# Kernel tuning notes

Hardware: AMD Instinct MI355X
Metric: run time of the kernel (lower is better)

## Reference

```python
import jax, jax.numpy as jnp
import numpy as np

B, N, C, H = 4, 1024, 768, 12
D = C // H  # head_dim = 64
EPS_BN = 1e-5


def setup_inputs() -> dict:
    key = jax.random.key(0)
    ks = jax.random.split(key, 8)
    s = np.float32(D ** -0.5)
    return {
        "x": jax.random.normal(ks[0], (B, N, C), dtype=jnp.float32),
        "qkv_w": jax.random.normal(ks[1], (3 * C, C), dtype=jnp.float32) * (C ** -0.5),
        "qkv_b": jnp.zeros((3 * C,), dtype=jnp.float32),
        "proj_w": jax.random.normal(ks[2], (C, C), dtype=jnp.float32) * (C ** -0.5),
        "proj_b": jnp.zeros((C,), dtype=jnp.float32),
        "scale": jnp.asarray(s),
        "riem_scale": jnp.asarray(s),
        "grass_scale": jnp.asarray(s),
        "conv_w": jax.random.normal(ks[3], (H, 3 * H), dtype=jnp.float32) * ((3 * H) ** -0.5),
        "conv_b": jnp.zeros((H,), dtype=jnp.float32),
        "bn_gamma": jnp.ones((H,), dtype=jnp.float32),
        "bn_beta": jnp.zeros((H,), dtype=jnp.float32),
        "bn_mean": jnp.zeros((H,), dtype=jnp.float32),
        "bn_var": jnp.ones((H,), dtype=jnp.float32),
    }


def reference(x, qkv_w, qkv_b, proj_w, proj_b, scale, riem_scale, grass_scale,
              conv_w, conv_b, bn_gamma, bn_beta, bn_mean, bn_var):
    Bx, Nx, Cx = x.shape
    # qkv projection -> [3, B, H, N, D]
    qkv = (x @ qkv_w.T + qkv_b).reshape(Bx, Nx, 3, H, D).transpose(2, 0, 3, 1, 4)
    q, k, v = qkv[0], qkv[1], qkv[2]

    # Grassmannian points: reduced QR over each [N, D] token matrix
    qgr, _ = jnp.linalg.qr(q)
    kgr, _ = jnp.linalg.qr(k)
    # dots [B,H,N,N]; norm over singleton dim == abs, then squared -> dots**2
    dots = jnp.einsum('bhnd,bhmd->bhnm', qgr, kgr)
    attn_grass = (dots * dots) * grass_scale

    # standard scaled dot-product scores
    qk = jnp.einsum('bhnd,bhmd->bhnm', q, k)
    attn = qk * scale

    # covariance Frobenius distance between rank-1 covariances q_i q_i^T, k_j k_j^T:
    # ||q q^T - k k^T||_F^2 = |q|^4 + |k|^4 - 2 (q.k)^2 ; similarity = -sqrt(.)
    qn2 = jnp.sum(q * q, axis=-1)  # [B,H,N]
    kn2 = jnp.sum(k * k, axis=-1)  # [B,H,N]
    d2 = qn2[..., :, None] ** 2 + kn2[..., None, :] ** 2 - 2.0 * (qk * qk)
    attn_riem = -jnp.sqrt(jnp.maximum(d2, 0.0) + 1e-8) * riem_scale

    # concat over head-channel dim -> [B, 3H, N, N], 1x1 conv + BatchNorm (eval stats)
    cat = jnp.concatenate([attn, attn_riem, attn_grass], axis=1)
    y = jnp.einsum('bcnm,oc->bonm', cat, conv_w) + conv_b[None, :, None, None]
    inv = (bn_gamma / jnp.sqrt(bn_var + EPS_BN))[None, :, None, None]
    y = (y - bn_mean[None, :, None, None]) * inv + bn_beta[None, :, None, None]

    p = jax.nn.softmax(y, axis=-1)
    out = jnp.einsum('bhnm,bhmd->bhnd', p, v)  # [B,H,N,D]
    out = out.transpose(0, 2, 1, 3).reshape(Bx, Nx, Cx)
    return out @ proj_w.T + proj_b
```

## Files before the change

kernel.cpp:

```cpp
#include <hip/hip_runtime.h>
#include <math.h>


typedef __attribute__((ext_vector_type(8))) short short8;
typedef __attribute__((ext_vector_type(4))) float f32x4;

__device__ __forceinline__ unsigned bf16r(float x) {
    unsigned u = __float_as_uint(x);
    return (u + 0x7FFFu + ((u >> 16) & 1u)) >> 16;
}
__device__ __forceinline__ unsigned packhl(float x) {
    unsigned u = __float_as_uint(x);
    unsigned hi = (u + 0x7FFFu + ((u >> 16) & 1u)) & 0xFFFF0000u;
    float lo = x - __uint_as_float(hi);
    unsigned ul = __float_as_uint(lo);
    unsigned l16 = (ul + 0x7FFFu + ((ul >> 16) & 1u)) >> 16;
    return hi | (l16 & 0xFFFFu);
}
__device__ __forceinline__ float unpackhl(unsigned u) {
    return __uint_as_float(u & 0xFFFF0000u) + __uint_as_float(u << 16);
}
union U4S8 { uint4 u; short8 s; };
__device__ __forceinline__ short8 mk_hi(uint4 a, uint4 b) {
    U4S8 r;
    r.u.x = __builtin_amdgcn_perm(a.y, a.x, 0x07060302);
    r.u.y = __builtin_amdgcn_perm(a.w, a.z, 0x07060302);
    r.u.z = __builtin_amdgcn_perm(b.y, b.x, 0x07060302);
    r.u.w = __builtin_amdgcn_perm(b.w, b.z, 0x07060302);
    return r.s;
}
__device__ __forceinline__ short8 mk_lo(uint4 a, uint4 b) {
    U4S8 r;
    r.u.x = __builtin_amdgcn_perm(a.y, a.x, 0x05040100);
    r.u.y = __builtin_amdgcn_perm(a.w, a.z, 0x05040100);
    r.u.z = __builtin_amdgcn_perm(b.y, b.x, 0x05040100);
    r.u.w = __builtin_amdgcn_perm(b.w, b.z, 0x05040100);
    return r.s;
}
__device__ __forceinline__ uint4 ld4v(const unsigned* vp, int mbase, int d) {
    uint4 r;
    r.x = vp[(size_t)(mbase + 0) * 64 + d];
    r.y = vp[(size_t)(mbase + 1) * 64 + d];
    r.z = vp[(size_t)(mbase + 2) * 64 + d];
    r.w = vp[(size_t)(mbase + 3) * 64 + d];
    return r;
}
#define MFMA(a,b,c) __builtin_amdgcn_mfma_f32_16x16x32_bf16(a, b, c, 0, 0, 0)

__global__ __launch_bounds__(256) void pack_f32(
    const float* __restrict__ src, unsigned* __restrict__ dst, int n4)
{
    int i = blockIdx.x * 256 + threadIdx.x;
    if (i < n4) {
        float4 v = *(const float4*)&src[(size_t)i * 4];
        uint4 o;
        o.x = packhl(v.x); o.y = packhl(v.y); o.z = packhl(v.z); o.w = packhl(v.w);
        *(uint4*)&dst[(size_t)i * 4] = o;
    }
}

__global__ __launch_bounds__(256) void qkv_mfma(
    const unsigned* __restrict__ xpk, const unsigned* __restrict__ wpk,
    const float* __restrict__ bias,
    float* __restrict__ q, float* __restrict__ k,
    unsigned* __restrict__ qpk, unsigned* __restrict__ kpk, unsigned* __restrict__ vpk)
{
    __shared__ unsigned xT[32 * 64];
    __shared__ unsigned wT[64 * 64];
    const int tid = threadIdx.x;
    const int lane = tid & 63;
    const int w = tid >> 6;
    const int rowL = lane & 15;
    const int g = lane >> 4;
    const int r7 = rowL & 7;
    const int n0 = blockIdx.x * 64;
    const int m0 = blockIdx.y * 32;
    f32x4 accA = {0,0,0,0}, accB = {0,0,0,0};

    for (int kk0 = 0; kk0 < 768; kk0 += 64) {
        __syncthreads();
#pragma unroll
        for (int e = 0; e < 2; e++) {
            int ci = tid + 256 * e; int R = ci >> 4, c = ci & 15;
            uint4 v = *(const uint4*)&xpk[(size_t)(m0 + R) * 768 + kk0 + c * 4];
            *(uint4*)&xT[R * 64 + ((c ^ (R & 7)) << 2)] = v;
        }
#pragma unroll
        for (int e = 0; e < 4; e++) {
            int ci = tid + 256 * e; int R = ci >> 4, c = ci & 15;
            uint4 v = *(const uint4*)&wpk[(size_t)(n0 + R) * 768 + kk0 + c * 4];
            *(uint4*)&wT[R * 64 + ((c ^ (R & 7)) << 2)] = v;
        }
        __syncthreads();
#pragma unroll
        for (int ks = 0; ks < 2; ks++) {
            int c0 = ks * 8 + g * 2;
            uint4 b0 = *(const uint4*)&wT[(w * 16 + rowL) * 64 + ((c0 ^ r7) << 2)];
            uint4 b1 = *(const uint4*)&wT[(w * 16 + rowL) * 64 + (((c0 + 1) ^ r7) << 2)];
            short8 whi = mk_hi(b0, b1), wlo = mk_lo(b0, b1);
            uint4 a0 = *(const uint4*)&xT[rowL * 64 + ((c0 ^ r7) << 2)];
            uint4 a1 = *(const uint4*)&xT[rowL * 64 + (((c0 + 1) ^ r7) << 2)];
            short8 xhi = mk_hi(a0, a1), xlo = mk_lo(a0, a1);
            accA = MFMA(xhi, whi, accA);
            accA = MFMA(xhi, wlo, accA);
            accA = MFMA(xlo, whi, accA);
            uint4 a2 = *(const uint4*)&xT[(16 + rowL) * 64 + ((c0 ^ r7) << 2)];
            uint4 a3 = *(const uint4*)&xT[(16 + rowL) * 64 + (((c0 + 1) ^ r7) << 2)];
            short8 xhi2 = mk_hi(a2, a3), xlo2 = mk_lo(a2, a3);
            accB = MFMA(xhi2, whi, accB);
            accB = MFMA(xhi2, wlo, accB);
            accB = MFMA(xlo2, whi, accB);
        }
    }
    const int col = n0 + w * 16 + rowL;
    const float bv = bias[col];
    const int s = (n0 >= 1536) ? 2 : ((n0 >= 768) ? 1 : 0);
    const int hc = col - s * 768;
    const int head = hc >> 6;
    const int cin = hc & 63;
#pragma unroll
    for (int half = 0; half < 2; half++) {
        f32x4 acc = half ? accB : accA;
#pragma unroll
        for (int r = 0; r < 4; r++) {
            int row = m0 + half * 16 + g * 4 + r;
            int bb = row >> 10, n = row & 1023;
            size_t idx = ((size_t)(bb * 12 + head) << 16) + ((size_t)n << 6) + cin;
            float val = acc[r] + bv;
            if (s == 0)      { q[idx] = val; qpk[idx] = packhl(val); }
            else if (s == 1) { k[idx] = val; kpk[idx] = packhl(val); }
            else             { vpk[idx] = packhl(val); }
        }
    }
}

__global__ __launch_bounds__(256) void proj_mfma(
    const unsigned* __restrict__ apk, const unsigned* __restrict__ wpk,
    const float* __restrict__ bias, float* __restrict__ out)
{
    __shared__ unsigned xT[32 * 64];
    __shared__ unsigned wT[64 * 64];
    const int tid = threadIdx.x;
    const int lane = tid & 63;
    const int w = tid >> 6;
    const int rowL = lane & 15;
    const int g = lane >> 4;
    const int r7 = rowL & 7;
    const int n0 = blockIdx.x * 64;
    const int m0 = blockIdx.y * 32;
    f32x4 accA = {0,0,0,0}, accB = {0,0,0,0};

    for (int kk0 = 0; kk0 < 768; kk0 += 64) {
        __syncthreads();
#pragma unroll
        for (int e = 0; e < 2; e++) {
            int ci = tid + 256 * e; int R = ci >> 4, c = ci & 15;
            uint4 v = *(const uint4*)&apk[(size_t)(m0 + R) * 768 + kk0 + c * 4];
            *(uint4*)&xT[R * 64 + ((c ^ (R & 7)) << 2)] = v;
        }
#pragma unroll
        for (int e = 0; e < 4; e++) {
            int ci = tid + 256 * e; int R = ci >> 4, c = ci & 15;
            uint4 v = *(const uint4*)&wpk[(size_t)(n0 + R) * 768 + kk0 + c * 4];
            *(uint4*)&wT[R * 64 + ((c ^ (R & 7)) << 2)] = v;
        }
        __syncthreads();
#pragma unroll
        for (int ks = 0; ks < 2; ks++) {
            int c0 = ks * 8 + g * 2;
            uint4 b0 = *(const uint4*)&wT[(w * 16 + rowL) * 64 + ((c0 ^ r7) << 2)];
            uint4 b1 = *(const uint4*)&wT[(w * 16 + rowL) * 64 + (((c0 + 1) ^ r7) << 2)];
            short8 whi = mk_hi(b0, b1), wlo = mk_lo(b0, b1);
            uint4 a0 = *(const uint4*)&xT[rowL * 64 + ((c0 ^ r7) << 2)];
            uint4 a1 = *(const uint4*)&xT[rowL * 64 + (((c0 + 1) ^ r7) << 2)];
            short8 xhi = mk_hi(a0, a1), xlo = mk_lo(a0, a1);
            accA = MFMA(xhi, whi, accA);
            accA = MFMA(xhi, wlo, accA);
            accA = MFMA(xlo, whi, accA);
            uint4 a2 = *(const uint4*)&xT[(16 + rowL) * 64 + ((c0 ^ r7) << 2)];
            uint4 a3 = *(const uint4*)&xT[(16 + rowL) * 64 + (((c0 + 1) ^ r7) << 2)];
            short8 xhi2 = mk_hi(a2, a3), xlo2 = mk_lo(a2, a3);
            accB = MFMA(xhi2, whi, accB);
            accB = MFMA(xhi2, wlo, accB);
            accB = MFMA(xlo2, whi, accB);
        }
    }
    const int col = n0 + w * 16 + rowL;
    const float bv = bias[col];
#pragma unroll
    for (int half = 0; half < 2; half++) {
        f32x4 acc = half ? accB : accA;
#pragma unroll
        for (int r = 0; r < 4; r++) {
            int row = m0 + half * 16 + g * 4 + r;
            out[(size_t)row * 768 + col] = acc[r] + bv;
        }
    }
}

__global__ __launch_bounds__(256) void qkv_gemm(
    const float* __restrict__ x, const float* __restrict__ w, const float* __restrict__ bias,
    float* __restrict__ q, float* __restrict__ k,
    unsigned* __restrict__ qpk, unsigned* __restrict__ kpk, unsigned* __restrict__ vpk)
{
    __shared__ float As[16][68];
    __shared__ float Ws[16][68];
    const int tid = threadIdx.x;
    const int m0 = blockIdx.x * 64;
    const int c0 = blockIdx.y * 64;
    const int ty = tid >> 4, tx = tid & 15;
    const int lm = tid >> 2;
    const int lk = (tid & 3) * 4;
    float acc[4][4];
#pragma unroll
    for (int i = 0; i < 4; i++)
#pragma unroll
        for (int j = 0; j < 4; j++) acc[i][j] = 0.f;

    for (int kk0 = 0; kk0 < 768; kk0 += 16) {
        float4 av = *(const float4*)&x[(m0 + lm) * 768 + kk0 + lk];
        float4 wv = *(const float4*)&w[(c0 + lm) * 768 + kk0 + lk];
        __syncthreads();
        As[lk + 0][lm] = av.x; As[lk + 1][lm] = av.y; As[lk + 2][lm] = av.z; As[lk + 3][lm] = av.w;
        Ws[lk + 0][lm] = wv.x; Ws[lk + 1][lm] = wv.y; Ws[lk + 2][lm] = wv.z; Ws[lk + 3][lm] = wv.w;
        __syncthreads();
#pragma unroll
        for (int kk = 0; kk < 16; kk++) {
            float4 a  = *(const float4*)&As[kk][ty * 4];
            float4 bv = *(const float4*)&Ws[kk][tx * 4];
            acc[0][0] += a.x * bv.x; acc[0][1] += a.x * bv.y; acc[0][2] += a.x * bv.z; acc[0][3] += a.x * bv.w;
            acc[1][0] += a.y * bv.x; acc[1][1] += a.y * bv.y; acc[1][2] += a.y * bv.z; acc[1][3] += a.y * bv.w;
            acc[2][0] += a.z * bv.x; acc[2][1] += a.z * bv.y; acc[2][2] += a.z * bv.z; acc[2][3] += a.z * bv.w;
            acc[3][0] += a.w * bv.x; acc[3][1] += a.w * bv.y; acc[3][2] += a.w * bv.z; acc[3][3] += a.w * bv.w;
        }
    }
#pragma unroll
    for (int i = 0; i < 4; i++) {
        int row = m0 + ty * 4 + i;
        int bb = row >> 10, n = row & 1023;
#pragma unroll
        for (int j = 0; j < 4; j++) {
            int col = c0 + tx * 4 + j;
            float val = acc[i][j] + bias[col];
            int s = (col >= 1536) ? 2 : ((col >= 768) ? 1 : 0);
            int hc = col - s * 768;
            size_t idx = ((size_t)(bb * 12 + (hc >> 6)) << 16) + ((size_t)n << 6) + (hc & 63);
            if (s == 0)      { q[idx] = val; qpk[idx] = packhl(val); }
            else if (s == 1) { k[idx] = val; kpk[idx] = packhl(val); }
            else             { vpk[idx] = packhl(val); }
        }
    }
}

__global__ __launch_bounds__(256) void row_norms(
    const float* __restrict__ q, const float* __restrict__ k,
    float* __restrict__ qn4, float* __restrict__ kn4)
{
    int wid = blockIdx.x * 4 + (threadIdx.x >> 6);
    int lane = threadIdx.x & 63;
    const float* src; float* dst; int r;
    if (wid < 49152) { src = q; dst = qn4; r = wid; }
    else             { src = k; dst = kn4; r = wid - 49152; }
    float xv = src[(size_t)r * 64 + lane];
    float s = xv * xv;
#pragma unroll
    for (int m = 1; m < 64; m <<= 1) s += __shfl_xor(s, m, 64);
    if (lane == 0) dst[r] = s * s;
}

__global__ __launch_bounds__(1024)
__attribute__((amdgpu_waves_per_eu(4, 4)))
void qr_fact(const float* __restrict__ q, const float* __restrict__ k,
             unsigned* __restrict__ Vp_, float* __restrict__ taug)
{
    const int id = blockIdx.x;
    const float* src = (id & 1) ? k : q;
    src += (size_t)(id >> 1) << 16;
    unsigned* Vp = Vp_ + (size_t)id * 65536;
    const int tid = threadIdx.x;
    const int lane = tid & 63;
    const int w = tid >> 6;
    __shared__ float vbufA[1024];
    __shared__ float vbufB[1024];
    __shared__ float taub[64];

    float a[4][16];
#pragma unroll
    for (int c = 0; c < 4; c++)
#pragma unroll
        for (int i = 0; i < 16; i++)
            a[c][i] = src[(i * 64 + lane) * 64 + 4 * w + c];

    if (w == 0) {
        float part = 0.f;
#pragma unroll
        for (int i = 0; i < 16; i++) part += a[0][i] * a[0][i];
#pragma unroll
        for (int m = 1; m < 64; m <<= 1) part += __shfl_xor(part, m, 64);
        float sigma = part;
        float xd = __shfl(a[0][0], 0, 64);
        float nrm = sqrtf(sigma);
        float beta = (xd >= 0.f) ? -nrm : nrm;
        float vd = xd - beta;
        float vtv = (sigma - xd * xd) + vd * vd;
        float tau2 = (vtv > 0.f) ? 2.f / vtv : 0.f;
        if (lane == 0) a[0][0] = vd;
#pragma unroll
        for (int i = 0; i < 16; i++) vbufA[i * 64 + lane] = a[0][i];
        if (lane == 0) taub[0] = tau2;
    }
    __syncthreads();

    for (int d = 0; d < 64; d++) {
        float* vb = (d & 1) ? vbufB : vbufA;
        float vr[16];
#pragma unroll
        for (int i = 0; i < 16; i++) vr[i] = vb[i * 64 + lane];
        float t2 = taub[d];
        float dp0 = 0.f, dp1 = 0.f, dp2 = 0.f, dp3 = 0.f;
#pragma unroll
        for (int i = 0; i < 16; i++) {
            dp0 += vr[i] * a[0][i];
            dp1 += vr[i] * a[1][i];
            dp2 += vr[i] * a[2][i];
            dp3 += vr[i] * a[3][i];
        }
#pragma unroll
        for (int m = 1; m < 64; m <<= 1) {
            dp0 += __shfl_xor(dp0, m, 64);
            dp1 += __shfl_xor(dp1, m, 64);
            dp2 += __shfl_xor(dp2, m, 64);
            dp3 += __shfl_xor(dp3, m, 64);
        }
        const int jb = 4 * w;
        float s0 = t2 * dp0, s1 = t2 * dp1, s2 = t2 * dp2, s3 = t2 * dp3;
        if (jb + 0 > d) {
#pragma unroll
            for (int i = 0; i < 16; i++) a[0][i] -= s0 * vr[i];
        }
        if (jb + 1 > d) {
#pragma unroll
            for (int i = 0; i < 16; i++) a[1][i] -= s1 * vr[i];
        }
        if (jb + 2 > d) {
#pragma unroll
            for (int i = 0; i < 16; i++) a[2][i] -= s2 * vr[i];
        }
        if (jb + 3 > d) {
#pragma unroll
            for (int i = 0; i < 16; i++) a[3][i] -= s3 * vr[i];
        }
        if (d < 63) {
            const int dn = d + 1;
            if (w == (dn >> 2)) {
                const int cd = dn & 3;
#pragma unroll
                for (int c = 0; c < 4; c++) if (c == cd) {
                    float part = 0.f;
#pragma unroll
                    for (int i = 0; i < 16; i++) {
                        int r = i * 64 + lane;
                        float xx = a[c][i];
                        part += (r >= dn) ? xx * xx : 0.f;
                    }
#pragma unroll
                    for (int m = 1; m < 64; m <<= 1) part += __shfl_xor(part, m, 64);
                    float sigma = part;
                    float xd = __shfl(a[c][0], dn, 64);
                    float nrm = sqrtf(sigma);
                    float beta = (xd >= 0.f) ? -nrm : nrm;
                    float vd = xd - beta;
                    float vtv = (sigma - xd * xd) + vd * vd;
                    float tau2 = (vtv > 0.f) ? 2.f / vtv : 0.f;
                    if (lane == dn) a[c][0] = vd;
                    float* vbn = (dn & 1) ? vbufB : vbufA;
#pragma unroll
                    for (int i = 0; i < 16; i++) {
                        int r = i * 64 + lane;
                        vbn[i * 64 + lane] = (r < dn) ? 0.f : a[c][i];
                    }
                    if (lane == 0) taub[dn] = tau2;
                }
            }
        }
        __syncthreads();
    }

    if (tid < 64) taug[id * 64 + tid] = taub[tid];
#pragma unroll
    for (int c = 0; c < 4; c++) {
        int j = 4 * w + c;
#pragma unroll
        for (int i = 0; i < 16; i++) {
            int r = i * 64 + lane;
            float vv = (r < j) ? 0.f : a[c][i];
            Vp[(size_t)j * 1024 + r] = packhl(vv);
        }
    }
}

__global__ __launch_bounds__(256) void qr_gpart(
    const unsigned* __restrict__ Vp_, float* __restrict__ Gpart)
{
    const int id = blockIdx.x;
    const int sl = blockIdx.y;
    const unsigned* Vp = Vp_ + (size_t)id * 65536;
    __shared__ unsigned Vc[64 * 32];
    const int tid = threadIdx.x;
    const int lane = tid & 63;
    const int w = tid >> 6;
    const int rowL = lane & 15;
    const int g = lane >> 4;

    f32x4 acc0 = {0,0,0,0}, acc1 = {0,0,0,0}, acc2 = {0,0,0,0}, acc3 = {0,0,0,0};
    for (int r0 = sl * 256; r0 < sl * 256 + 256; r0 += 32) {
        __syncthreads();
#pragma unroll
        for (int e = 0; e < 2; e++) {
            int ci = tid + 256 * e;
            int row = ci >> 3, c = ci & 7;
            uint4 v = *(const uint4*)&Vp[(size_t)row * 1024 + r0 + c * 4];
            *(uint4*)&Vc[row * 32 + ((c ^ (row & 7)) << 2)] = v;
        }
        __syncthreads();
        int ra = w * 16 + rowL;
        uint4 a0 = *(const uint4*)&Vc[ra * 32 + (((g * 2) ^ (ra & 7)) << 2)];
        uint4 a1 = *(const uint4*)&Vc[ra * 32 + (((g * 2 + 1) ^ (ra & 7)) << 2)];
        short8 Ahi = mk_hi(a0, a1), Alo = mk_lo(a0, a1);
#define GDO(jt, accv) { int rb = jt * 16 + rowL; \
        uint4 b0 = *(const uint4*)&Vc[rb * 32 + (((g * 2) ^ (rb & 7)) << 2)]; \
        uint4 b1 = *(const uint4*)&Vc[rb * 32 + (((g * 2 + 1) ^ (rb & 7)) << 2)]; \
        short8 Bhi = mk_hi(b0, b1), Blo = mk_lo(b0, b1); \
        accv = MFMA(Ahi, Bhi, accv); accv = MFMA(Ahi, Blo, accv); accv = MFMA(Alo, Bhi, accv); }
        GDO(0, acc0) GDO(1, acc1) GDO(2, acc2) GDO(3, acc3)
#undef GDO
    }
    float* dst = Gpart + ((size_t)(id * 4 + sl) << 12);
#define GWR(jt, accv) { \
    dst[(w * 16 + g * 4 + 0) * 64 + jt * 16 + rowL] = accv[0]; \
    dst[(w * 16 + g * 4 + 1) * 64 + jt * 16 + rowL] = accv[1]; \
    dst[(w * 16 + g * 4 + 2) * 64 + jt * 16 + rowL] = accv[2]; \
    dst[(w * 16 + g * 4 + 3) * 64 + jt * 16 + rowL] = accv[3]; }
    GWR(0, acc0) GWR(1, acc1) GWR(2, acc2) GWR(3, acc3)
#undef GWR
}

__global__ __launch_bounds__(256) void qr_tw2(
    const unsigned* __restrict__ Vp_, const float* __restrict__ taug,
    const float* __restrict__ Gpart, float* __restrict__ Wg)
{
    const int id = blockIdx.x;
    const unsigned* Vp = Vp_ + (size_t)id * 65536;
    __shared__ float G_s[64 * 65];
    __shared__ float wbuf[64];
    __shared__ float tau_s[64];
    const int tid = threadIdx.x;
    if (tid < 64) tau_s[tid] = taug[id * 64 + tid];
    const float* Gp = Gpart + ((size_t)(id * 4) << 12);
#pragma unroll
    for (int e = 0; e < 16; e++) {
        int idx = tid + 256 * e;
        float sum = Gp[idx] + Gp[4096 + idx] + Gp[8192 + idx] + Gp[12288 + idx];
        G_s[(idx >> 6) * 65 + (idx & 63)] = sum;
    }
    const int i = tid >> 2;
    const int cq = tid & 3;
    float regA[16];
#pragma unroll
    for (int cc = 0; cc < 16; cc++)
        regA[cc] = unpackhl(Vp[(size_t)i * 1024 + cq * 16 + cc]);
    __syncthreads();
    for (int j = 63; j >= 0; j--) {
        if (i == j) {
            float tj = tau_s[j];
#pragma unroll
            for (int cc = 0; cc < 16; cc++) {
                regA[cc] *= tj;
                wbuf[cq * 16 + cc] = regA[cc];
            }
        }
        __syncthreads();
        if (i < j) {
            float gij = G_s[i * 65 + j];
#pragma unroll
            for (int cc = 0; cc < 16; cc++)
                regA[cc] = fmaf(-gij, wbuf[cq * 16 + cc], regA[cc]);
        }
        __syncthreads();
    }
#pragma unroll
    for (int cc = 0; cc < 16; cc++)
        Wg[(size_t)id * 4096 + i * 64 + cq * 16 + cc] = regA[cc];
}

__global__ __launch_bounds__(256) void qr_formq(
    const unsigned* __restrict__ Vp_, const float* __restrict__ Wg,
    unsigned short* __restrict__ qgrh, unsigned short* __restrict__ kgrh)
{
    const int id = blockIdx.x;
    const int rb = blockIdx.y;
    const unsigned* Vp = Vp_ + (size_t)id * 65536;
    const float* Wm = Wg + (size_t)id * 4096;
    unsigned short* dst = ((id & 1) ? kgrh : qgrh) + ((size_t)(id >> 1) << 16);
    __shared__ float Vl[64 * 65];
    __shared__ float Wl[64 * 64];
    const int tid = threadIdx.x;
    const int rbase = rb * 64;
#pragma unroll
    for (int e = 0; e < 16; e++) {
        int idx = tid + 256 * e;
        int j = idx >> 6, rl = idx & 63;
        Vl[rl * 65 + j] = unpackhl(Vp[(size_t)j * 1024 + rbase + rl]);
        Wl[idx] = Wm[idx];
    }
    __syncthreads();
    const int rl = tid >> 2;
    const int cg = (tid & 3) << 4;
    const int rglob = rbase + rl;
    unsigned short outv[16];
#pragma unroll
    for (int cc = 0; cc < 16; cc++) {
        int c = cg + cc;
        float s = (rglob == c) ? 1.f : 0.f;
        for (int j = 0; j < 64; j++) s -= Vl[rl * 65 + j] * Wl[j * 64 + c];
        outv[cc] = (unsigned short)bf16r(s);
    }
#pragma unroll
    for (int cc = 0; cc < 16; cc += 4)
        *(ushort4*)&dst[(size_t)rglob * 64 + cg + cc] = *(ushort4*)&outv[cc];
}

#define SC_EACH12(F) F(0) F(1) F(2) F(3) F(4) F(5) F(6) F(7) F(8) F(9) F(10) F(11)
#define SC_DECLY(o) float y##o##_0 = 0.f, y##o##_1 = 0.f, y##o##_2 = 0.f, y##o##_3 = 0.f;
#define SC_LOADC(o) const float cA##o = cw[o * 36 + h], \
                                cB##o = cw[o * 36 + 12 + h], \
                                cC##o = cw[o * 36 + 24 + h];
#define SC_CONV1(o,r) y##o##_##r = fmaf(cA##o, att, fmaf(cB##o, rie, fmaf(cC##o, gra, y##o##_##r)));
#define SC_CONVROW(r) SC_CONV1(0,r) SC_CONV1(1,r) SC_CONV1(2,r) SC_CONV1(3,r) SC_CONV1(4,r) SC_CONV1(5,r) \
                      SC_CONV1(6,r) SC_CONV1(7,r) SC_CONV1(8,r) SC_CONV1(9,r) SC_CONV1(10,r) SC_CONV1(11,r)
#define SC_SCORE(r) { \
    float qk = s1[r], gr = s2[r]; \
    float qn4v = qn4s[g * 4 + r]; \
    float att = qk * scale; \
    float d2 = qn4v + kn4v - 2.f * qk * qk; \
    float rie = -sqrtf(fmaxf(d2, 0.f) + 1e-8f) * riem_scale; \
    float gra = gr * gr * grass_scale; \
    SC_CONVROW(r) }
#define SC_OUT(o) { \
    float inv = bn_gamma[o] * rsqrtf(bn_var[o] + 1e-5f); \
    float Bb = fmaf(conv_b[o] - bn_mean[o], inv, bn_beta[o]); \
    float* dst = Sbuf + ((size_t)(z * 12 + o) * 1024 + n0) * 1024 + m0 + w * 16 + rowL; \
    dst[(size_t)(g * 4 + 0) * 1024] = fmaf(y##o##_0, inv, Bb); \
    dst[(size_t)(g * 4 + 1) * 1024] = fmaf(y##o##_1, inv, Bb); \
    dst[(size_t)(g * 4 + 2) * 1024] = fmaf(y##o##_2, inv, Bb); \
    dst[(size_t)(g * 4 + 3) * 1024] = fmaf(y##o##_3, inv, Bb); }

__global__ __launch_bounds__(256) void sattn_scores(
    const unsigned* __restrict__ qpk, const unsigned* __restrict__ kpk,
    const unsigned short* __restrict__ qgrh, const unsigned short* __restrict__ kgrh,
    const float* __restrict__ qn4g, const float* __restrict__ kn4g,
    const float* __restrict__ cw, const float* __restrict__ conv_b,
    const float* __restrict__ bn_gamma, const float* __restrict__ bn_beta,
    const float* __restrict__ bn_mean, const float* __restrict__ bn_var,
    const float* __restrict__ scale_p, const float* __restrict__ riem_p,
    const float* __restrict__ grass_p, float* __restrict__ Sbuf, int b0)
{
    __shared__ unsigned qT[16 * 64];
    __shared__ unsigned short qgT[16 * 64];
    __shared__ unsigned kL[64 * 64];
    __shared__ unsigned short kgrL[64 * 64];
    __shared__ float qn4s[16];
    __shared__ float kn4s[64];

    const int tid = threadIdx.x;
    const int lane = tid & 63;
    const int w = tid >> 6;
    const int rowL = lane & 15;
    const int g = lane >> 4;
    const int r7 = rowL & 7;
    const int m0 = blockIdx.x * 64;
    const int n0 = blockIdx.y * 16;
    const int z = blockIdx.z;
    const int b = b0 + z;
    const float scale = scale_p[0], riem_scale = riem_p[0], grass_scale = grass_p[0];

    SC_EACH12(SC_DECLY)

    for (int h = 0; h < 12; h++) {
        __syncthreads();
        {
            int R = tid >> 4, c = tid & 15;
            uint4 v = *(const uint4*)&qpk[((size_t)(b * 12 + h) << 16) + (size_t)(n0 + R) * 64 + c * 4];
            *(uint4*)&qT[R * 64 + ((c ^ (R & 7)) << 2)] = v;
        }
        if (tid < 128) {
            int R = tid >> 3, c = tid & 7;
            uint4 v = *(const uint4*)&qgrh[((size_t)(b * 12 + h) << 16) + (size_t)(n0 + R) * 64 + c * 8];
            *(uint4*)&qgT[R * 64 + ((c ^ (R & 7)) << 3)] = v;
        }
#pragma unroll
        for (int e = 0; e < 4; e++) {
            int ci = tid + 256 * e; int m = ci >> 4, c = ci & 15;
            uint4 v = *(const uint4*)&kpk[((size_t)(b * 12 + h) << 16) + (size_t)(m0 + m) * 64 + c * 4];
            *(uint4*)&kL[m * 64 + ((c ^ (m & 7)) << 2)] = v;
        }
#pragma unroll
        for (int e = 0; e < 2; e++) {
            int ci = tid + 256 * e; int m = ci >> 3, c = ci & 7;
            uint4 v = *(const uint4*)&kgrh[((size_t)(b * 12 + h) << 16) + (size_t)(m0 + m) * 64 + c * 8];
            *(uint4*)&kgrL[m * 64 + ((c ^ (m & 7)) << 3)] = v;
        }
        if (tid < 64) kn4s[tid] = kn4g[(size_t)(b * 12 + h) * 1024 + m0 + tid];
        if (tid < 16) qn4s[tid] = qn4g[(size_t)(b * 12 + h) * 1024 + n0 + tid];
        __syncthreads();

        float kn4v = kn4s[w * 16 + rowL];
        f32x4 s1 = {0,0,0,0}, s2 = {0,0,0,0};
#pragma unroll
        for (int ks = 0; ks < 2; ks++) {
            int c0 = ks * 8 + g * 2;
            uint4 a0 = *(const uint4*)&qT[rowL * 64 + ((c0 ^ r7) << 2)];
            uint4 a1 = *(const uint4*)&qT[rowL * 64 + (((c0 + 1) ^ r7) << 2)];
            uint4 b0v = *(const uint4*)&kL[(w * 16 + rowL) * 64 + ((c0 ^ r7) << 2)];
            uint4 b1v = *(const uint4*)&kL[(w * 16 + rowL) * 64 + (((c0 + 1) ^ r7) << 2)];
            short8 qhi = mk_hi(a0, a1), qlo = mk_lo(a0, a1);
            short8 khi = mk_hi(b0v, b1v), klo = mk_lo(b0v, b1v);
            s1 = MFMA(qhi, khi, s1);
            s1 = MFMA(qhi, klo, s1);
            s1 = MFMA(qlo, khi, s1);
            int cg = ks * 4 + g;
            short8 qg = *(const short8*)&qgT[rowL * 64 + ((cg ^ r7) << 3)];
            short8 kg2 = *(const short8*)&kgrL[(w * 16 + rowL) * 64 + ((cg ^ r7) << 3)];
            s2 = MFMA(qg, kg2, s2);
        }
        SC_EACH12(SC_LOADC)
        SC_SCORE(0) SC_SCORE(1) SC_SCORE(2) SC_SCORE(3)
    }
    SC_EACH12(SC_OUT)
}

__global__ __launch_bounds__(256) void sattn_pv(
    const unsigned* __restrict__ vpk, const float* __restrict__ Sbuf,
    void* __restrict__ attno_out, int b0, int packout)
{
    __shared__ unsigned short P_s[16 * 64];
    __shared__ unsigned vt_s[64 * 64];
    __shared__ float mrun[16], lrun[16], cos_[16];

    const int tid = threadIdx.x;
    const int lane = tid & 63;
    const int w = tid >> 6;
    const int rowL = lane & 15;
    const int g = lane >> 4;
    const int r7 = rowL & 7;
    const int n0 = blockIdx.x * 16;
    const int o = blockIdx.y;
    const int z = blockIdx.z;
    const int b = b0 + z;
    const int srow = tid >> 4;
    const int sc4 = (tid & 15) * 4;

    if (tid < 16) { mrun[tid] = -1e30f; lrun[tid] = 0.f; }
    f32x4 acc = {0,0,0,0};
    const float* Srow = Sbuf + ((size_t)(z * 12 + o) * 1024 + n0 + srow) * 1024;
    const unsigned* vp = vpk + ((size_t)(b * 12 + o) << 16);
    __syncthreads();

    for (int m0 = 0; m0 < 1024; m0 += 64) {
        float4 sv = *(const float4*)&Srow[m0 + sc4];
        float mx = fmaxf(fmaxf(sv.x, sv.y), fmaxf(sv.z, sv.w));
        mx = fmaxf(mx, __shfl_xor(mx, 1, 64));
        mx = fmaxf(mx, __shfl_xor(mx, 2, 64));
        mx = fmaxf(mx, __shfl_xor(mx, 4, 64));
        mx = fmaxf(mx, __shfl_xor(mx, 8, 64));
        float mo = mrun[srow];
        float mn = fmaxf(mo, mx);
        float co = expf(mo - mn);
        float p0 = expf(sv.x - mn), p1 = expf(sv.y - mn), p2 = expf(sv.z - mn), p3 = expf(sv.w - mn);
        unsigned u0 = bf16r(p0), u1 = bf16r(p1), u2 = bf16r(p2), u3 = bf16r(p3);
        {
            ushort4 pw = make_ushort4((unsigned short)u0, (unsigned short)u1,
                                      (unsigned short)u2, (unsigned short)u3);
            *(ushort4*)&P_s[srow * 64 + (((sc4 >> 3) ^ (srow & 7)) << 3) + (sc4 & 7)] = pw;
        }
        float ps = __uint_as_float(u0 << 16) + __uint_as_float(u1 << 16)
                 + __uint_as_float(u2 << 16) + __uint_as_float(u3 << 16);
        ps += __shfl_xor(ps, 1, 64); ps += __shfl_xor(ps, 2, 64);
        ps += __shfl_xor(ps, 4, 64); ps += __shfl_xor(ps, 8, 64);
        if ((lane & 15) == 0) {
            mrun[srow] = mn;
            cos_[srow] = co;
            lrun[srow] = lrun[srow] * co + ps;
        }
#pragma unroll
        for (int e = 0; e < 4; e++) {
            int d_ = tid & 63;
            int mb = (tid >> 6) * 4 + 16 * e;
            int mc = (tid >> 6) + 4 * e;
            uint4 v = ld4v(vp + (size_t)m0 * 64, mb, d_);
            *(uint4*)&vt_s[d_ * 64 + ((mc ^ (d_ & 15)) << 2)] = v;
        }
        __syncthreads();
        {
            float c0_ = cos_[g * 4 + 0], c1_ = cos_[g * 4 + 1];
            float c2_ = cos_[g * 4 + 2], c3_ = cos_[g * 4 + 3];
            acc[0] *= c0_; acc[1] *= c1_; acc[2] *= c2_; acc[3] *= c3_;
        }
        const int d_ = w * 16 + rowL;
        const unsigned* vrow = &vt_s[d_ * 64];
#pragma unroll
        for (int kk = 0; kk < 2; kk++) {
            int mc8 = kk * 4 + g;
            short8 pa = *(const short8*)&P_s[rowL * 64 + ((mc8 ^ r7) << 3)];
            int c0 = kk * 8 + g * 2;
            uint4 b0v = *(const uint4*)&vrow[((c0 ^ (d_ & 15)) << 2)];
            uint4 b1v = *(const uint4*)&vrow[(((c0 + 1) ^ (d_ & 15)) << 2)];
            short8 vh = mk_hi(b0v, b1v), vl = mk_lo(b0v, b1v);
            acc = MFMA(pa, vh, acc);
            acc = MFMA(pa, vl, acc);
        }
        __syncthreads();
    }
#pragma unroll
    for (int r = 0; r < 4; r++) {
        int row = g * 4 + r;
        size_t idx = ((size_t)(b * 1024 + n0 + row)) * 768 + o * 64 + w * 16 + rowL;
        float v = acc[r] / lrun[row];
        if (packout) ((unsigned*)attno_out)[idx] = packhl(v);
        else         ((float*)attno_out)[idx] = v;
    }
}

__global__ __launch_bounds__(256) void proj_gemm(
    const float* __restrict__ x, const float* __restrict__ w, const float* __restrict__ bias,
    float* __restrict__ out)
{
    __shared__ float As[16][68];
    __shared__ float Ws[16][68];
    const int tid = threadIdx.x;
    const int m0 = blockIdx.x * 64;
    const int c0 = blockIdx.y * 64;
    const int ty = tid >> 4, tx = tid & 15;
    const int lm = tid >> 2;
    const int lk = (tid & 3) * 4;
    float acc[4][4];
#pragma unroll
    for (int i = 0; i < 4; i++)
#pragma unroll
        for (int j = 0; j < 4; j++) acc[i][j] = 0.f;

    for (int kk0 = 0; kk0 < 768; kk0 += 16) {
        float4 av = *(const float4*)&x[(m0 + lm) * 768 + kk0 + lk];
        float4 wv = *(const float4*)&w[(c0 + lm) * 768 + kk0 + lk];
        __syncthreads();
        As[lk + 0][lm] = av.x; As[lk + 1][lm] = av.y; As[lk + 2][lm] = av.z; As[lk + 3][lm] = av.w;
        Ws[lk + 0][lm] = wv.x; Ws[lk + 1][lm] = wv.y; Ws[lk + 2][lm] = wv.z; Ws[lk + 3][lm] = wv.w;
        __syncthreads();
#pragma unroll
        for (int kk = 0; kk < 16; kk++) {
            float4 a  = *(const float4*)&As[kk][ty * 4];
            float4 bv = *(const float4*)&Ws[kk][tx * 4];
            acc[0][0] += a.x * bv.x; acc[0][1] += a.x * bv.y; acc[0][2] += a.x * bv.z; acc[0][3] += a.x * bv.w;
            acc[1][0] += a.y * bv.x; acc[1][1] += a.y * bv.y; acc[1][2] += a.y * bv.z; acc[1][3] += a.y * bv.w;
            acc[2][0] += a.z * bv.x; acc[2][1] += a.z * bv.y; acc[2][2] += a.z * bv.z; acc[2][3] += a.z * bv.w;
            acc[3][0] += a.w * bv.x; acc[3][1] += a.w * bv.y; acc[3][2] += a.w * bv.z; acc[3][3] += a.w * bv.w;
        }
    }
#pragma unroll
    for (int i = 0; i < 4; i++) {
        int row = m0 + ty * 4 + i;
#pragma unroll
        for (int j = 0; j < 4; j++) {
            int col = c0 + tx * 4 + j;
            out[(size_t)row * 768 + col] = acc[i][j] + bias[col];
        }
    }
}

extern "C" void kernel_launch(void* const* d_in, const int* in_sizes, int n_in,
                              void* d_out, int out_size, void* d_ws, size_t ws_size,
                              hipStream_t stream) {
    const float* x          = (const float*)d_in[0];
    const float* qkv_w      = (const float*)d_in[1];
    const float* qkv_b      = (const float*)d_in[2];
    const float* proj_w     = (const float*)d_in[3];
    const float* proj_b     = (const float*)d_in[4];
    const float* scale      = (const float*)d_in[5];
    const float* riem_scale = (const float*)d_in[6];
    const float* grass_scale= (const float*)d_in[7];
    const float* conv_w     = (const float*)d_in[8];
    const float* conv_b     = (const float*)d_in[9];
    const float* bn_gamma   = (const float*)d_in[10];
    const float* bn_beta    = (const float*)d_in[11];
    const float* bn_mean    = (const float*)d_in[12];
    const float* bn_var     = (const float*)d_in[13];
    float* out = (float*)d_out;

    float* q   = (float*)d_ws;
    float* k   = q + 3145728;
    unsigned* qpk = (unsigned*)(k + 3145728);
    unsigned* kpk = qpk + 3145728;
    unsigned* vpk = kpk + 3145728;
    unsigned short* qgrh = (unsigned short*)(vpk + 3145728);
    unsigned short* kgrh = qgrh + 3145728;
    float* qn4 = (float*)(kgrh + 3145728);
    float* kn4 = qn4 + 49152;
    float* attno = q;
    unsigned* attno_pk = (unsigned*)q;
    unsigned* ppk = (unsigned*)k;

    const size_t BASE = 75890688ull;
    const size_t SB1  = 50331648ull;
    float* Sbuf = (float*)((char*)d_ws + BASE);
    unsigned* xpk_ = (unsigned*)((char*)d_ws + BASE);
    unsigned* wpk_ = xpk_ + 3145728;
    unsigned* Vpk2 = (unsigned*)((char*)d_ws + BASE);
    float* Wg   = (float*)(Vpk2 + 96 * 65536);
    float* taug = Wg + 96 * 4096;
    float* Gpart = taug + 96 * 64;
    const bool havePk = (ws_size >= BASE + SB1);
    const bool full   = (ws_size >= BASE + 4 * SB1);

    if (havePk) {
        hipLaunchKernelGGL(pack_f32, dim3(3072), dim3(256), 0, stream, x, xpk_, 786432);
        hipLaunchKernelGGL(pack_f32, dim3(1728), dim3(256), 0, stream, qkv_w, wpk_, 442368);
        hipLaunchKernelGGL(qkv_mfma, dim3(36, 128), dim3(256), 0, stream,
                           xpk_, wpk_, qkv_b, q, k, qpk, kpk, vpk);
    } else {
        hipLaunchKernelGGL(qkv_gemm, dim3(64, 36), dim3(256), 0, stream,
                           x, qkv_w, qkv_b, q, k, qpk, kpk, vpk);
    }
    hipLaunchKernelGGL(row_norms, dim3(24576), dim3(256), 0, stream, q, k, qn4, kn4);

    hipLaunchKernelGGL(qr_fact, dim3(96), dim3(1024), 0, stream, q, k, Vpk2, taug);
    hipLaunchKernelGGL(qr_gpart, dim3(96, 4), dim3(256), 0, stream, Vpk2, Gpart);
    hipLaunchKernelGGL(qr_tw2, dim3(96), dim3(256), 0, stream, Vpk2, taug, Gpart, Wg);
    hipLaunchKernelGGL(qr_formq, dim3(96, 16), dim3(256), 0, stream, Vpk2, Wg, qgrh, kgrh);

    if (havePk)
        hipLaunchKernelGGL(pack_f32, dim3(576), dim3(256), 0, stream, proj_w, ppk, 147456);

    if (full) {
        hipLaunchKernelGGL(sattn_scores, dim3(16, 64, 4), dim3(256), 0, stream,
                           qpk, kpk, qgrh, kgrh, qn4, kn4, conv_w, conv_b,
                           bn_gamma, bn_beta, bn_mean, bn_var,
                           scale, riem_scale, grass_scale, Sbuf, 0);
        hipLaunchKernelGGL(sattn_pv, dim3(64, 12, 4), dim3(256), 0, stream,
                           vpk, Sbuf, (void*)attno_pk, 0, 1);
    } else {
        for (int b = 0; b < 4; b++) {
            hipLaunchKernelGGL(sattn_scores, dim3(16, 64, 1), dim3(256), 0, stream,
                               qpk, kpk, qgrh, kgrh, qn4, kn4, conv_w, conv_b,
                               bn_gamma, bn_beta, bn_mean, bn_var,
                               scale, riem_scale, grass_scale, Sbuf, b);
            hipLaunchKernelGGL(sattn_pv, dim3(64, 12, 1), dim3(256), 0, stream,
                               vpk, Sbuf, (void*)(havePk ? (void*)attno_pk : (void*)attno), b,
                               havePk ? 1 : 0);
        }
    }

    if (havePk) {
        hipLaunchKernelGGL(proj_mfma, dim3(12, 128), dim3(256), 0, stream,
                           attno_pk, ppk, proj_b, out);
    } else {
        hipLaunchKernelGGL(proj_gemm, dim3(64, 12), dim3(256), 0, stream,
                           attno, proj_w, proj_b, out);
    }
}
```

Baseline: 678.8 us.

## Fuse fp32-to-bf16 split packing into GEMM loads and skip finished QR columns

```diff
diff --git a/kernel.cpp b/kernel.cpp
--- a/kernel.cpp
+++ b/kernel.cpp
@@ -16,6 +16,11 @@
     unsigned ul = __float_as_uint(lo);
     unsigned l16 = (ul + 0x7FFFu + ((ul >> 16) & 1u)) >> 16;
     return hi | (l16 & 0xFFFFu);
+}
+__device__ __forceinline__ uint4 pack4(float4 v) {
+    uint4 o;
+    o.x = packhl(v.x); o.y = packhl(v.y); o.z = packhl(v.z); o.w = packhl(v.w);
+    return o;
 }
 __device__ __forceinline__ float unpackhl(unsigned u) {
     return __uint_as_float(u & 0xFFFF0000u) + __uint_as_float(u << 16);
@@ -47,20 +52,8 @@
 }
 #define MFMA(a,b,c) __builtin_amdgcn_mfma_f32_16x16x32_bf16(a, b, c, 0, 0, 0)
 
-__global__ __launch_bounds__(256) void pack_f32(
-    const float* __restrict__ src, unsigned* __restrict__ dst, int n4)
-{
-    int i = blockIdx.x * 256 + threadIdx.x;
-    if (i < n4) {
-        float4 v = *(const float4*)&src[(size_t)i * 4];
-        uint4 o;
-        o.x = packhl(v.x); o.y = packhl(v.y); o.z = packhl(v.z); o.w = packhl(v.w);
-        *(uint4*)&dst[(size_t)i * 4] = o;
-    }
-}
-
 __global__ __launch_bounds__(256) void qkv_mfma(
-    const unsigned* __restrict__ xpk, const unsigned* __restrict__ wpk,
+    const float* __restrict__ x, const float* __restrict__ wsrc,
     const float* __restrict__ bias,
     float* __restrict__ q, float* __restrict__ k,
     unsigned* __restrict__ qpk, unsigned* __restrict__ kpk, unsigned* __restrict__ vpk)
@@ -82,14 +75,14 @@
 #pragma unroll
         for (int e = 0; e < 2; e++) {
             int ci = tid + 256 * e; int R = ci >> 4, c = ci & 15;
-            uint4 v = *(const uint4*)&xpk[(size_t)(m0 + R) * 768 + kk0 + c * 4];
-            *(uint4*)&xT[R * 64 + ((c ^ (R & 7)) << 2)] = v;
+            float4 fv = *(const float4*)&x[(size_t)(m0 + R) * 768 + kk0 + c * 4];
+            *(uint4*)&xT[R * 64 + ((c ^ (R & 7)) << 2)] = pack4(fv);
         }
 #pragma unroll
         for (int e = 0; e < 4; e++) {
             int ci = tid + 256 * e; int R = ci >> 4, c = ci & 15;
-            uint4 v = *(const uint4*)&wpk[(size_t)(n0 + R) * 768 + kk0 + c * 4];
-            *(uint4*)&wT[R * 64 + ((c ^ (R & 7)) << 2)] = v;
+            float4 fv = *(const float4*)&wsrc[(size_t)(n0 + R) * 768 + kk0 + c * 4];
+            *(uint4*)&wT[R * 64 + ((c ^ (R & 7)) << 2)] = pack4(fv);
         }
         __syncthreads();
 #pragma unroll
@@ -135,7 +128,7 @@
 }
 
 __global__ __launch_bounds__(256) void proj_mfma(
-    const unsigned* __restrict__ apk, const unsigned* __restrict__ wpk,
+    const unsigned* __restrict__ apk, const float* __restrict__ wsrc,
     const float* __restrict__ bias, float* __restrict__ out)
 {
     __shared__ unsigned xT[32 * 64];
@@ -161,8 +154,8 @@
 #pragma unroll
         for (int e = 0; e < 4; e++) {
             int ci = tid + 256 * e; int R = ci >> 4, c = ci & 15;
-            uint4 v = *(const uint4*)&wpk[(size_t)(n0 + R) * 768 + kk0 + c * 4];
-            *(uint4*)&wT[R * 64 + ((c ^ (R & 7)) << 2)] = v;
+            float4 fv = *(const float4*)&wsrc[(size_t)(n0 + R) * 768 + kk0 + c * 4];
+            *(uint4*)&wT[R * 64 + ((c ^ (R & 7)) << 2)] = pack4(fv);
         }
         __syncthreads();
 #pragma unroll
@@ -198,60 +191,6 @@
     }
 }
 
-__global__ __launch_bounds__(256) void qkv_gemm(
-    const float* __restrict__ x, const float* __restrict__ w, const float* __restrict__ bias,
-    float* __restrict__ q, float* __restrict__ k,
-    unsigned* __restrict__ qpk, unsigned* __restrict__ kpk, unsigned* __restrict__ vpk)
-{
-    __shared__ float As[16][68];
-    __shared__ float Ws[16][68];
-    const int tid = threadIdx.x;
-    const int m0 = blockIdx.x * 64;
-    const int c0 = blockIdx.y * 64;
-    const int ty = tid >> 4, tx = tid & 15;
-    const int lm = tid >> 2;
-    const int lk = (tid & 3) * 4;
-    float acc[4][4];
-#pragma unroll
-    for (int i = 0; i < 4; i++)
-#pragma unroll
-        for (int j = 0; j < 4; j++) acc[i][j] = 0.f;
-
-    for (int kk0 = 0; kk0 < 768; kk0 += 16) {
-        float4 av = *(const float4*)&x[(m0 + lm) * 768 + kk0 + lk];
-        float4 wv = *(const float4*)&w[(c0 + lm) * 768 + kk0 + lk];
-        __syncthreads();
-        As[lk + 0][lm] = av.x; As[lk + 1][lm] = av.y; As[lk + 2][lm] = av.z; As[lk + 3][lm] = av.w;
-        Ws[lk + 0][lm] = wv.x; Ws[lk + 1][lm] = wv.y; Ws[lk + 2][lm] = wv.z; Ws[lk + 3][lm] = wv.w;
-        __syncthreads();
-#pragma unroll
-        for (int kk = 0; kk < 16; kk++) {
-            float4 a  = *(const float4*)&As[kk][ty * 4];
-            float4 bv = *(const float4*)&Ws[kk][tx * 4];
-            acc[0][0] += a.x * bv.x; acc[0][1] += a.x * bv.y; acc[0][2] += a.x * bv.z; acc[0][3] += a.x * bv.w;
-            acc[1][0] += a.y * bv.x; acc[1][1] += a.y * bv.y; acc[1][2] += a.y * bv.z; acc[1][3] += a.y * bv.w;
-            acc[2][0] += a.z * bv.x; acc[2][1] += a.z * bv.y; acc[2][2] += a.z * bv.z; acc[2][3] += a.z * bv.w;
-            acc[3][0] += a.w * bv.x; acc[3][1] += a.w * bv.y; acc[3][2] += a.w * bv.z; acc[3][3] += a.w * bv.w;
-        }
-    }
-#pragma unroll
-    for (int i = 0; i < 4; i++) {
-        int row = m0 + ty * 4 + i;
-        int bb = row >> 10, n = row & 1023;
-#pragma unroll
-        for (int j = 0; j < 4; j++) {
-            int col = c0 + tx * 4 + j;
-            float val = acc[i][j] + bias[col];
-            int s = (col >= 1536) ? 2 : ((col >= 768) ? 1 : 0);
-            int hc = col - s * 768;
-            size_t idx = ((size_t)(bb * 12 + (hc >> 6)) << 16) + ((size_t)n << 6) + (hc & 63);
-            if (s == 0)      { q[idx] = val; qpk[idx] = packhl(val); }
-            else if (s == 1) { k[idx] = val; kpk[idx] = packhl(val); }
-            else             { vpk[idx] = packhl(val); }
-        }
-    }
-}
-
 __global__ __launch_bounds__(256) void row_norms(
     const float* __restrict__ q, const float* __restrict__ k,
     float* __restrict__ qn4, float* __restrict__ kn4)
@@ -312,43 +251,45 @@
     __syncthreads();
 
     for (int d = 0; d < 64; d++) {
-        float* vb = (d & 1) ? vbufB : vbufA;
-        float vr[16];
-#pragma unroll
-        for (int i = 0; i < 16; i++) vr[i] = vb[i * 64 + lane];
-        float t2 = taub[d];
-        float dp0 = 0.f, dp1 = 0.f, dp2 = 0.f, dp3 = 0.f;
-#pragma unroll
-        for (int i = 0; i < 16; i++) {
-            dp0 += vr[i] * a[0][i];
-            dp1 += vr[i] * a[1][i];
-            dp2 += vr[i] * a[2][i];
-            dp3 += vr[i] * a[3][i];
-        }
-#pragma unroll
-        for (int m = 1; m < 64; m <<= 1) {
-            dp0 += __shfl_xor(dp0, m, 64);
-            dp1 += __shfl_xor(dp1, m, 64);
-            dp2 += __shfl_xor(dp2, m, 64);
-            dp3 += __shfl_xor(dp3, m, 64);
-        }
         const int jb = 4 * w;
-        float s0 = t2 * dp0, s1 = t2 * dp1, s2 = t2 * dp2, s3 = t2 * dp3;
-        if (jb + 0 > d) {
-#pragma unroll
-            for (int i = 0; i < 16; i++) a[0][i] -= s0 * vr[i];
-        }
-        if (jb + 1 > d) {
-#pragma unroll
-            for (int i = 0; i < 16; i++) a[1][i] -= s1 * vr[i];
-        }
-        if (jb + 2 > d) {
-#pragma unroll
-            for (int i = 0; i < 16; i++) a[2][i] -= s2 * vr[i];
-        }
         if (jb + 3 > d) {
-#pragma unroll
-            for (int i = 0; i < 16; i++) a[3][i] -= s3 * vr[i];
+            float* vb = (d & 1) ? vbufB : vbufA;
+            float vr[16];
+#pragma unroll
+            for (int i = 0; i < 16; i++) vr[i] = vb[i * 64 + lane];
+            float t2 = taub[d];
+            float dp0 = 0.f, dp1 = 0.f, dp2 = 0.f, dp3 = 0.f;
+#pragma unroll
+            for (int i = 0; i < 16; i++) {
+                dp0 += vr[i] * a[0][i];
+                dp1 += vr[i] * a[1][i];
+                dp2 += vr[i] * a[2][i];
+                dp3 += vr[i] * a[3][i];
+            }
+#pragma unroll
+            for (int m = 1; m < 64; m <<= 1) {
+                dp0 += __shfl_xor(dp0, m, 64);
+                dp1 += __shfl_xor(dp1, m, 64);
+                dp2 += __shfl_xor(dp2, m, 64);
+                dp3 += __shfl_xor(dp3, m, 64);
+            }
+            float s0 = t2 * dp0, s1 = t2 * dp1, s2 = t2 * dp2, s3 = t2 * dp3;
+            if (jb + 0 > d) {
+#pragma unroll
+                for (int i = 0; i < 16; i++) a[0][i] -= s0 * vr[i];
+            }
+            if (jb + 1 > d) {
+#pragma unroll
+                for (int i = 0; i < 16; i++) a[1][i] -= s1 * vr[i];
+            }
+            if (jb + 2 > d) {
+#pragma unroll
+                for (int i = 0; i < 16; i++) a[2][i] -= s2 * vr[i];
+            }
+            {
+#pragma unroll
+                for (int i = 0; i < 16; i++) a[3][i] -= s3 * vr[i];
+            }
         }
         if (d < 63) {
             const int dn = d + 1;
@@ -641,7 +582,7 @@
 
 __global__ __launch_bounds__(256) void sattn_pv(
     const unsigned* __restrict__ vpk, const float* __restrict__ Sbuf,
-    void* __restrict__ attno_out, int b0, int packout)
+    unsigned* __restrict__ attno_pk, int b0)
 {
     __shared__ unsigned short P_s[16 * 64];
     __shared__ unsigned vt_s[64 * 64];
@@ -725,55 +666,7 @@
     for (int r = 0; r < 4; r++) {
         int row = g * 4 + r;
         size_t idx = ((size_t)(b * 1024 + n0 + row)) * 768 + o * 64 + w * 16 + rowL;
-        float v = acc[r] / lrun[row];
-        if (packout) ((unsigned*)attno_out)[idx] = packhl(v);
-        else         ((float*)attno_out)[idx] = v;
-    }
-}
-
-__global__ __launch_bounds__(256) void proj_gemm(
-    const float* __restrict__ x, const float* __restrict__ w, const float* __restrict__ bias,
-    float* __restrict__ out)
-{
-    __shared__ float As[16][68];
-    __shared__ float Ws[16][68];
-    const int tid = threadIdx.x;
-    const int m0 = blockIdx.x * 64;
-    const int c0 = blockIdx.y * 64;
-    const int ty = tid >> 4, tx = tid & 15;
-    const int lm = tid >> 2;
-    const int lk = (tid & 3) * 4;
-    float acc[4][4];
-#pragma unroll
-    for (int i = 0; i < 4; i++)
-#pragma unroll
-        for (int j = 0; j < 4; j++) acc[i][j] = 0.f;
-
-    for (int kk0 = 0; kk0 < 768; kk0 += 16) {
-        float4 av = *(const float4*)&x[(m0 + lm) * 768 + kk0 + lk];
-        float4 wv = *(const float4*)&w[(c0 + lm) * 768 + kk0 + lk];
-        __syncthreads();
-        As[lk + 0][lm] = av.x; As[lk + 1][lm] = av.y; As[lk + 2][lm] = av.z; As[lk + 3][lm] = av.w;
-        Ws[lk + 0][lm] = wv.x; Ws[lk + 1][lm] = wv.y; Ws[lk + 2][lm] = wv.z; Ws[lk + 3][lm] = wv.w;
-        __syncthreads();
-#pragma unroll
-        for (int kk = 0; kk < 16; kk++) {
-            float4 a  = *(const float4*)&As[kk][ty * 4];
-            float4 bv = *(const float4*)&Ws[kk][tx * 4];
-            acc[0][0] += a.x * bv.x; acc[0][1] += a.x * bv.y; acc[0][2] += a.x * bv.z; acc[0][3] += a.x * bv.w;
-            acc[1][0] += a.y * bv.x; acc[1][1] += a.y * bv.y; acc[1][2] += a.y * bv.z; acc[1][3] += a.y * bv.w;
-            acc[2][0] += a.z * bv.x; acc[2][1] += a.z * bv.y; acc[2][2] += a.z * bv.z; acc[2][3] += a.z * bv.w;
-            acc[3][0] += a.w * bv.x; acc[3][1] += a.w * bv.y; acc[3][2] += a.w * bv.z; acc[3][3] += a.w * bv.w;
-        }
-    }
-#pragma unroll
-    for (int i = 0; i < 4; i++) {
-        int row = m0 + ty * 4 + i;
-#pragma unroll
-        for (int j = 0; j < 4; j++) {
-            int col = c0 + tx * 4 + j;
-            out[(size_t)row * 768 + col] = acc[i][j] + bias[col];
-        }
+        attno_pk[idx] = packhl(acc[r] / lrun[row]);
     }
 }
 
@@ -805,40 +698,25 @@
     unsigned short* kgrh = qgrh + 3145728;
     float* qn4 = (float*)(kgrh + 3145728);
     float* kn4 = qn4 + 49152;
-    float* attno = q;
     unsigned* attno_pk = (unsigned*)q;
-    unsigned* ppk = (unsigned*)k;
 
     const size_t BASE = 75890688ull;
     const size_t SB1  = 50331648ull;
     float* Sbuf = (float*)((char*)d_ws + BASE);
-    unsigned* xpk_ = (unsigned*)((char*)d_ws + BASE);
-    unsigned* wpk_ = xpk_ + 3145728;
     unsigned* Vpk2 = (unsigned*)((char*)d_ws + BASE);
     float* Wg   = (float*)(Vpk2 + 96 * 65536);
     float* taug = Wg + 96 * 4096;
     float* Gpart = taug + 96 * 64;
-    const bool havePk = (ws_size >= BASE + SB1);
-    const bool full   = (ws_size >= BASE + 4 * SB1);
-
-    if (havePk) {
-        hipLaunchKernelGGL(pack_f32, dim3(3072), dim3(256), 0, stream, x, xpk_, 786432);
-        hipLaunchKernelGGL(pack_f32, dim3(1728), dim3(256), 0, stream, qkv_w, wpk_, 442368);
-        hipLaunchKernelGGL(qkv_mfma, dim3(36, 128), dim3(256), 0, stream,
-                           xpk_, wpk_, qkv_b, q, k, qpk, kpk, vpk);
-    } else {
-        hipLaunchKernelGGL(qkv_gemm, dim3(64, 36), dim3(256), 0, stream,
-                           x, qkv_w, qkv_b, q, k, qpk, kpk, vpk);
-    }
+    const bool full = (ws_size >= BASE + 4 * SB1);
+
+    hipLaunchKernelGGL(qkv_mfma, dim3(36, 128), dim3(256), 0, stream,
+                       x, qkv_w, qkv_b, q, k, qpk, kpk, vpk);
     hipLaunchKernelGGL(row_norms, dim3(24576), dim3(256), 0, stream, q, k, qn4, kn4);
 
     hipLaunchKernelGGL(qr_fact, dim3(96), dim3(1024), 0, stream, q, k, Vpk2, taug);
     hipLaunchKernelGGL(qr_gpart, dim3(96, 4), dim3(256), 0, stream, Vpk2, Gpart);
     hipLaunchKernelGGL(qr_tw2, dim3(96), dim3(256), 0, stream, Vpk2, taug, Gpart, Wg);
     hipLaunchKernelGGL(qr_formq, dim3(96, 16), dim3(256), 0, stream, Vpk2, Wg, qgrh, kgrh);
-
-    if (havePk)
-        hipLaunchKernelGGL(pack_f32, dim3(576), dim3(256), 0, stream, proj_w, ppk, 147456);
 
     if (full) {
         hipLaunchKernelGGL(sattn_scores, dim3(16, 64, 4), dim3(256), 0, stream,
@@ -846,7 +724,7 @@
                            bn_gamma, bn_beta, bn_mean, bn_var,
                            scale, riem_scale, grass_scale, Sbuf, 0);
         hipLaunchKernelGGL(sattn_pv, dim3(64, 12, 4), dim3(256), 0, stream,
-                           vpk, Sbuf, (void*)attno_pk, 0, 1);
+                           vpk, Sbuf, attno_pk, 0);
     } else {
         for (int b = 0; b < 4; b++) {
             hipLaunchKernelGGL(sattn_scores, dim3(16, 64, 1), dim3(256), 0, stream,
@@ -854,16 +732,10 @@
                                bn_gamma, bn_beta, bn_mean, bn_var,
                                scale, riem_scale, grass_scale, Sbuf, b);
             hipLaunchKernelGGL(sattn_pv, dim3(64, 12, 1), dim3(256), 0, stream,
-                               vpk, Sbuf, (void*)(havePk ? (void*)attno_pk : (void*)attno), b,
-                               havePk ? 1 : 0);
-        }
-    }
-
-    if (havePk) {
-        hipLaunchKernelGGL(proj_mfma, dim3(12, 128), dim3(256), 0, stream,
-                           attno_pk, ppk, proj_b, out);
-    } else {
-        hipLaunchKernelGGL(proj_gemm, dim3(64, 12), dim3(256), 0, stream,
-                           attno, proj_w, proj_b, out);
-    }
-}
+                               vpk, Sbuf, attno_pk, b);
+        }
+    }
+
+    hipLaunchKernelGGL(proj_mfma, dim3(12, 128), dim3(256), 0, stream,
+                       attno_pk, proj_w, proj_b, out);
+}
```

After: 683.2 us. Within noise of the previous version (+0.6%).
